# Optimization experiments

Measured on AMD Instinct MI355X. Metric: run time of the kernel, lower is better.

## Reference

```python
import jax, jax.numpy as jnp
import numpy as np

N_NODES = 100000
N_EDGES = 600000
N_RELS = 500
D = 128
RRELU_SLOPE = (1.0 / 8.0 + 1.0 / 3.0) / 2.0  # nn.RReLU eval-mode fixed slope


def setup_inputs() -> dict:
    key = jax.random.key(0)
    ks = jax.random.split(key, 9)
    ent_embed = jax.random.normal(ks[0], (N_NODES, D), dtype=jnp.float32)
    rel_embed = jax.random.normal(ks[1], (N_RELS, D), dtype=jnp.float32)
    W_rel0 = jax.random.normal(ks[2], (D, D), dtype=jnp.float32) * 0.05
    W_loop0 = jax.random.normal(ks[3], (D, D), dtype=jnp.float32) * 0.05
    W_rel1 = jax.random.normal(ks[4], (D, D), dtype=jnp.float32) * 0.05
    W_loop1 = jax.random.normal(ks[5], (D, D), dtype=jnp.float32) * 0.05
    src = jax.random.randint(ks[6], (N_EDGES,), 0, N_NODES, dtype=jnp.int32)
    dst = jax.random.randint(ks[7], (N_EDGES,), 0, N_NODES, dtype=jnp.int32)
    rel_id = jax.random.randint(ks[8], (N_EDGES,), 0, N_RELS, dtype=jnp.int32)
    # standard DGL right-norm: 1 / in-degree per destination node
    deg = jnp.zeros((N_NODES,), dtype=jnp.float32).at[dst].add(1.0)
    norm = (1.0 / jnp.maximum(deg, 1.0))[:, None]  # (N, 1)
    return {
        "ent_embed": ent_embed, "rel_embed": rel_embed, "norm": norm,
        "W_rel0": W_rel0, "W_loop0": W_loop0,
        "W_rel1": W_rel1, "W_loop1": W_loop1,
        "src": src, "dst": dst, "rel_id": rel_id,
    }


def reference(ent_embed, rel_embed, norm, W_rel0, W_loop0, W_rel1, W_loop1, src, dst, rel_id):
    n = ent_embed.shape[0]
    edge_h = rel_embed[rel_id]  # (E, D), set once, reused across layers (as in source)
    h = ent_embed
    for W_rel, W_loop in ((W_rel0, W_loop0), (W_rel1, W_loop1)):
        self_msg = h @ W_loop                      # (N, D)
        msg = (edge_h + h[src]) @ W_rel            # gather src + edge, transform
        agg = jax.ops.segment_sum(msg, dst, num_segments=n)  # scatter-sum to dst
        h = jax.nn.leaky_relu(agg * norm + self_msg, RRELU_SLOPE)
    return h
```

## Files before the change

### kernel.cpp

```cpp
#include <hip/hip_runtime.h>
#include <hip/hip_bf16.h>

#define NN 100000
#define NE 600000
#define DD 128
#define SLOPE 0.22916666666666666f
#define NB1 98
#define SENT ((500u << 17) | 100000u)
#define MAXSLOT 1000448
#define NTILE 6250

typedef __attribute__((ext_vector_type(4))) float f32x4;
typedef __attribute__((ext_vector_type(4))) unsigned u32x4;
typedef __attribute__((ext_vector_type(8))) short s16x8;
typedef __attribute__((ext_vector_type(4))) short s16x4;

__device__ __forceinline__ unsigned short f2b(float f) {
  union { float f; unsigned u; } v; v.f = f;
  unsigned u = v.u;
  return (unsigned short)((u + 0x7fffu + ((u >> 16) & 1u)) >> 16);
}
__device__ __forceinline__ float b2f(short s) {
  union { unsigned u; float f; } v;
  v.u = ((unsigned)(unsigned short)s) << 16;
  return v.f;
}
__device__ __forceinline__ int pdegf(float nm) {
  int d = (int)(1.0f / nm + 0.5f);
  return (d + 3) & ~3;
}

__global__ void prep_all(const float* __restrict__ ent, const float* __restrict__ rel,
                         const float* __restrict__ Wr0, const float* __restrict__ Wl0,
                         const float* __restrict__ Wr1, const float* __restrict__ Wl1,
                         unsigned short* __restrict__ entb, unsigned short* __restrict__ relb,
                         unsigned short* __restrict__ Wt) {
  int i = blockIdx.x * blockDim.x + threadIdx.x;
  if (i < (NN + 1) * 16) {
    s16x8 o = {0, 0, 0, 0, 0, 0, 0, 0};
    if (i < NN * 16) {
      f32x4 v0 = *(const f32x4*)(ent + (size_t)i * 8);
      f32x4 v1 = *(const f32x4*)(ent + (size_t)i * 8 + 4);
      o[0] = (short)f2b(v0[0]); o[1] = (short)f2b(v0[1]);
      o[2] = (short)f2b(v0[2]); o[3] = (short)f2b(v0[3]);
      o[4] = (short)f2b(v1[0]); o[5] = (short)f2b(v1[1]);
      o[6] = (short)f2b(v1[2]); o[7] = (short)f2b(v1[3]);
    }
    *(s16x8*)(entb + (size_t)i * 8) = o;
  }
  if (i < 501 * 16) {
    s16x8 o = {0, 0, 0, 0, 0, 0, 0, 0};
    if (i < 500 * 16) {
      f32x4 v0 = *(const f32x4*)(rel + (size_t)i * 8);
      f32x4 v1 = *(const f32x4*)(rel + (size_t)i * 8 + 4);
      o[0] = (short)f2b(v0[0]); o[1] = (short)f2b(v0[1]);
      o[2] = (short)f2b(v0[2]); o[3] = (short)f2b(v0[3]);
      o[4] = (short)f2b(v1[0]); o[5] = (short)f2b(v1[1]);
      o[6] = (short)f2b(v1[2]); o[7] = (short)f2b(v1[3]);
    }
    *(s16x8*)(relb + (size_t)i * 8) = o;
  }
  if (i < 8192) {
    int L = i >> 12, rem = i & 4095;
    int n = rem >> 9, k = (rem >> 6) & 7, lane = rem & 63;
    int c = n * 16 + (lane & 15);
    int kk0 = k * 32 + (lane >> 4) * 8;
    const float* Wr = L ? Wr1 : Wr0;
    const float* Wl = L ? Wl1 : Wl0;
    s16x8 o;
#pragma unroll
    for (int t = 0; t < 8; t++) {
      int kk = kk0 + t;
      float v = (kk < DD) ? Wr[kk * DD + c] : Wl[(kk - DD) * DD + c];
      o[t] = (short)f2b(v);
    }
    *(s16x8*)(Wt + (size_t)i * 8) = o;
  }
}

__global__ void sentinel_fill(unsigned* __restrict__ epack) {
  int i = blockIdx.x * blockDim.x + threadIdx.x;
  if (i < MAXSLOT / 4) {
    u32x4 s = {SENT, SENT, SENT, SENT};
    *(u32x4*)(epack + (size_t)i * 4) = s;
  }
}

__global__ void scan_a(const float* __restrict__ norm, int* __restrict__ psum) {
  __shared__ int lds[256];
  int b = blockIdx.x, t = threadIdx.x;
  int base = b * 1024 + t * 4;
  int s = 0;
#pragma unroll
  for (int j = 0; j < 4; j++) { int i = base + j; if (i < NN) s += pdegf(norm[i]); }
  lds[t] = s; __syncthreads();
  for (int st = 128; st > 0; st >>= 1) { if (t < st) lds[t] += lds[t + st]; __syncthreads(); }
  if (t == 0) psum[b] = lds[0];
}

__global__ void scan_b(int* __restrict__ psum, int* __restrict__ off) {
  __shared__ int lds[128];
  int t = threadIdx.x;
  lds[t] = (t < NB1) ? psum[t] : 0; __syncthreads();
  for (int st = 1; st < 128; st <<= 1) {
    int v = (t >= st) ? lds[t - st] : 0;
    __syncthreads();
    lds[t] += v;
    __syncthreads();
  }
  if (t == 127) off[NN] = lds[127];
  if (t < NB1) psum[t] = t ? lds[t - 1] : 0;
}

__global__ void scan_c(const float* __restrict__ norm, const int* __restrict__ psum,
                       int* __restrict__ off, int* __restrict__ cur) {
  __shared__ int lds[256];
  int b = blockIdx.x, t = threadIdx.x;
  int base = b * 1024 + t * 4;
  int v[4]; int s = 0;
#pragma unroll
  for (int j = 0; j < 4; j++) { int i = base + j; v[j] = (i < NN) ? pdegf(norm[i]) : 0; s += v[j]; }
  lds[t] = s; __syncthreads();
  for (int st = 1; st < 256; st <<= 1) {
    int u = (t >= st) ? lds[t - st] : 0;
    __syncthreads();
    lds[t] += u;
    __syncthreads();
  }
  int run = (t ? lds[t - 1] : 0) + psum[b];
#pragma unroll
  for (int j = 0; j < 4; j++) {
    int i = base + j;
    if (i < NN) { off[i] = run; cur[i] = run; run += v[j]; }
  }
}

__global__ void fill_pack(const int* __restrict__ src, const int* __restrict__ dst,
                          const int* __restrict__ rid, int* __restrict__ cur,
                          unsigned* __restrict__ epack) {
  int e = blockIdx.x * blockDim.x + threadIdx.x;
  if (e < NE) {
    int slot = atomicAdd(&cur[dst[e]], 1);
    epack[slot] = (unsigned)src[e] | ((unsigned)rid[e] << 17);
  }
}

__global__ void gather1(const unsigned short* __restrict__ hb, const unsigned short* __restrict__ relb,
                        const float* __restrict__ norm, const int* __restrict__ off,
                        const unsigned* __restrict__ epack,
                        unsigned short* __restrict__ preb, unsigned short* __restrict__ relaggn) {
  int gid = blockIdx.x * blockDim.x + threadIdx.x;
  int g = gid >> 5;
  if (g >= NN) return;
  int c = (gid & 31) << 2;
  int beg = off[g], end = off[g + 1];
  float h0 = 0.f, h1 = 0.f, h2 = 0.f, h3 = 0.f;
  float r0 = 0.f, r1 = 0.f, r2 = 0.f, r3 = 0.f;
  for (int e = beg; e < end; e += 4) {
    u32x4 w = *(const u32x4*)(epack + e);
    s16x4 hv[4], rv[4];
#pragma unroll
    for (int j = 0; j < 4; j++) {
      int s = (int)(w[j] & 0x1FFFFu);
      int r = (int)(w[j] >> 17);
      hv[j] = *(const s16x4*)(hb + (size_t)s * DD + c);
      rv[j] = *(const s16x4*)(relb + (size_t)r * DD + c);
    }
#pragma unroll
    for (int j = 0; j < 4; j++) {
      h0 += b2f(hv[j][0]); h1 += b2f(hv[j][1]);
      h2 += b2f(hv[j][2]); h3 += b2f(hv[j][3]);
      r0 += b2f(rv[j][0]); r1 += b2f(rv[j][1]);
      r2 += b2f(rv[j][2]); r3 += b2f(rv[j][3]);
    }
  }
  float nm = norm[g];
  s16x4 p, q;
  p[0] = (short)f2b((h0 + r0) * nm); p[1] = (short)f2b((h1 + r1) * nm);
  p[2] = (short)f2b((h2 + r2) * nm); p[3] = (short)f2b((h3 + r3) * nm);
  q[0] = (short)f2b(r0 * nm); q[1] = (short)f2b(r1 * nm);
  q[2] = (short)f2b(r2 * nm); q[3] = (short)f2b(r3 * nm);
  *(s16x4*)(preb + (size_t)g * DD + c) = p;
  *(s16x4*)(relaggn + (size_t)g * DD + c) = q;
}

__global__ void gather2(const unsigned short* __restrict__ hb, const unsigned short* __restrict__ relaggn,
                        const float* __restrict__ norm, const int* __restrict__ off,
                        const unsigned* __restrict__ epack, unsigned short* __restrict__ preb) {
  int gid = blockIdx.x * blockDim.x + threadIdx.x;
  int g = gid >> 5;
  if (g >= NN) return;
  int c = (gid & 31) << 2;
  int beg = off[g], end = off[g + 1];
  float h0 = 0.f, h1 = 0.f, h2 = 0.f, h3 = 0.f;
  for (int e = beg; e < end; e += 4) {
    u32x4 w = *(const u32x4*)(epack + e);
    s16x4 hv[4];
#pragma unroll
    for (int j = 0; j < 4; j++) {
      int s = (int)(w[j] & 0x1FFFFu);
      hv[j] = *(const s16x4*)(hb + (size_t)s * DD + c);
    }
#pragma unroll
    for (int j = 0; j < 4; j++) {
      h0 += b2f(hv[j][0]); h1 += b2f(hv[j][1]);
      h2 += b2f(hv[j][2]); h3 += b2f(hv[j][3]);
    }
  }
  float nm = norm[g];
  s16x4 ra = *(const s16x4*)(relaggn + (size_t)g * DD + c);
  s16x4 p;
  p[0] = (short)f2b(__builtin_fmaf(h0, nm, b2f(ra[0])));
  p[1] = (short)f2b(__builtin_fmaf(h1, nm, b2f(ra[1])));
  p[2] = (short)f2b(__builtin_fmaf(h2, nm, b2f(ra[2])));
  p[3] = (short)f2b(__builtin_fmaf(h3, nm, b2f(ra[3])));
  *(s16x4*)(preb + (size_t)g * DD + c) = p;
}

template <int OUTF32>
__launch_bounds__(512, 4)
__global__ void layer_mm(const unsigned short* __restrict__ preb, const unsigned short* __restrict__ hb,
                         const unsigned short* __restrict__ Wt, void* __restrict__ outp) {
  __shared__ unsigned short Blds[32768];
  int tid = threadIdx.x;
  int wave = tid >> 6, lane = tid & 63;
  int l16 = lane & 15, lhi = lane >> 4;

  for (int i = tid; i < 4096; i += 512)
    *(s16x8*)(&Blds[(size_t)i * 8]) = *(const s16x8*)(Wt + (size_t)i * 8);
  __syncthreads();

  const unsigned short* Bl = &Blds[lane * 8];

  int gw = blockIdx.x * 8 + wave;
  int t0 = gw, t1 = gw + 4096;
  bool has1 = t1 < NTILE;

  const unsigned short* Ap0 = preb + (size_t)(t0 * 16 + l16) * DD + lhi * 8;
  const unsigned short* Ah0 = hb + (size_t)(t0 * 16 + l16) * DD + lhi * 8;
  s16x8 a0[8], a1[8];
#pragma unroll
  for (int ks = 0; ks < 4; ks++) a0[ks] = *(const s16x8*)(Ap0 + ks * 32);
#pragma unroll
  for (int ks = 0; ks < 4; ks++) a0[4 + ks] = *(const s16x8*)(Ah0 + ks * 32);
  if (has1) {
    const unsigned short* Ap1 = preb + (size_t)(t1 * 16 + l16) * DD + lhi * 8;
    const unsigned short* Ah1 = hb + (size_t)(t1 * 16 + l16) * DD + lhi * 8;
#pragma unroll
    for (int ks = 0; ks < 4; ks++) a1[ks] = *(const s16x8*)(Ap1 + ks * 32);
#pragma unroll
    for (int ks = 0; ks < 4; ks++) a1[4 + ks] = *(const s16x8*)(Ah1 + ks * 32);
  }

  {
    f32x4 acc[8];
#pragma unroll
    for (int n = 0; n < 8; n++) acc[n] = (f32x4){0.f, 0.f, 0.f, 0.f};
#pragma unroll
    for (int n = 0; n < 8; n++) {
#pragma unroll
      for (int k = 0; k < 8; k++) {
        s16x8 b = *(const s16x8*)(Bl + (n * 8 + k) * 512);
        acc[n] = __builtin_amdgcn_mfma_f32_16x16x32_bf16(a0[k], b, acc[n], 0, 0, 0);
      }
    }
    int r0 = t0 * 16;
#pragma unroll
    for (int n = 0; n < 8; n++) {
#pragma unroll
      for (int j = 0; j < 4; j++) {
        int gr = r0 + lhi * 4 + j;
        float x = acc[n][j];
        x = x > 0.f ? x : x * SLOPE;
        if (OUTF32) ((float*)outp)[(size_t)gr * DD + n * 16 + l16] = x;
        else ((unsigned short*)outp)[(size_t)gr * DD + n * 16 + l16] = f2b(x);
      }
    }
  }
  if (has1) {
    f32x4 acc[8];
#pragma unroll
    for (int n = 0; n < 8; n++) acc[n] = (f32x4){0.f, 0.f, 0.f, 0.f};
#pragma unroll
    for (int n = 0; n < 8; n++) {
#pragma unroll
      for (int k = 0; k < 8; k++) {
        s16x8 b = *(const s16x8*)(Bl + (n * 8 + k) * 512);
        acc[n] = __builtin_amdgcn_mfma_f32_16x16x32_bf16(a1[k], b, acc[n], 0, 0, 0);
      }
    }
    int r0 = t1 * 16;
#pragma unroll
    for (int n = 0; n < 8; n++) {
#pragma unroll
      for (int j = 0; j < 4; j++) {
        int gr = r0 + lhi * 4 + j;
        float x = acc[n][j];
        x = x > 0.f ? x : x * SLOPE;
        if (OUTF32) ((float*)outp)[(size_t)gr * DD + n * 16 + l16] = x;
        else ((unsigned short*)outp)[(size_t)gr * DD + n * 16 + l16] = f2b(x);
      }
    }
  }
}

extern "C" void kernel_launch(void* const* d_in, const int* in_sizes, int n_in,
                              void* d_out, int out_size, void* d_ws, size_t ws_size,
                              hipStream_t stream) {
  const float* ent  = (const float*)d_in[0];
  const float* rel  = (const float*)d_in[1];
  const float* norm = (const float*)d_in[2];
  const float* Wr0  = (const float*)d_in[3];
  const float* Wl0  = (const float*)d_in[4];
  const float* Wr1  = (const float*)d_in[5];
  const float* Wl1  = (const float*)d_in[6];
  const int* src = (const int*)d_in[7];
  const int* dst = (const int*)d_in[8];
  const int* rid = (const int*)d_in[9];
  float* out = (float*)d_out;

  char* ws = (char*)d_ws;
  unsigned short* entb    = (unsigned short*)ws;
  unsigned short* preb    = (unsigned short*)(ws + 25600256);
  unsigned short* relaggn = (unsigned short*)(ws + 51200256);
  unsigned short* Wt      = (unsigned short*)(ws + 76800256);
  unsigned short* relb    = (unsigned short*)(ws + 76931328);
  int* off   = (int*)(ws + 77059584);
  int* cur   = (int*)(ws + 77459600);
  int* psum  = (int*)(ws + 77859600);
  unsigned* epack = (unsigned*)(ws + 77860112);

  prep_all<<<((NN + 1) * 16 + 255) / 256, 256, 0, stream>>>(ent, rel, Wr0, Wl0, Wr1, Wl1, entb, relb, Wt);
  sentinel_fill<<<(MAXSLOT / 4 + 255) / 256, 256, 0, stream>>>(epack);

  scan_a<<<NB1, 256, 0, stream>>>(norm, psum);
  scan_b<<<1, 128, 0, stream>>>(psum, off);
  scan_c<<<NB1, 256, 0, stream>>>(norm, psum, off, cur);
  fill_pack<<<(NE + 255) / 256, 256, 0, stream>>>(src, dst, rid, cur, epack);

  const int gb = (NN * 32 + 255) / 256;

  gather1<<<gb, 256, 0, stream>>>(entb, relb, norm, off, epack, preb, relaggn);
  layer_mm<0><<<512, 512, 0, stream>>>(preb, entb, Wt, entb);

  gather2<<<gb, 256, 0, stream>>>(entb, relaggn, norm, off, epack, preb);
  layer_mm<1><<<512, 512, 0, stream>>>(preb, entb, Wt + 32768, out);
}
```

Before: 171.4 us.

## Build CSR edge list via atomicExch linked lists instead of atomic-add slots

```diff
diff --git a/kernel.cpp b/kernel.cpp
--- a/kernel.cpp
+++ b/kernel.cpp
@@ -78,14 +78,6 @@
   }
 }
 
-__global__ void sentinel_fill(unsigned* __restrict__ epack) {
-  int i = blockIdx.x * blockDim.x + threadIdx.x;
-  if (i < MAXSLOT / 4) {
-    u32x4 s = {SENT, SENT, SENT, SENT};
-    *(u32x4*)(epack + (size_t)i * 4) = s;
-  }
-}
-
 __global__ void scan_a(const float* __restrict__ norm, int* __restrict__ psum) {
   __shared__ int lds[256];
   int b = blockIdx.x, t = threadIdx.x;
@@ -113,7 +105,7 @@
 }
 
 __global__ void scan_c(const float* __restrict__ norm, const int* __restrict__ psum,
-                       int* __restrict__ off, int* __restrict__ cur) {
+                       int* __restrict__ off) {
   __shared__ int lds[256];
   int b = blockIdx.x, t = threadIdx.x;
   int base = b * 1024 + t * 4;
@@ -131,18 +123,35 @@
 #pragma unroll
   for (int j = 0; j < 4; j++) {
     int i = base + j;
-    if (i < NN) { off[i] = run; cur[i] = run; run += v[j]; }
-  }
-}
-
-__global__ void fill_pack(const int* __restrict__ src, const int* __restrict__ dst,
-                          const int* __restrict__ rid, int* __restrict__ cur,
-                          unsigned* __restrict__ epack) {
-  int e = blockIdx.x * blockDim.x + threadIdx.x;
-  if (e < NE) {
-    int slot = atomicAdd(&cur[dst[e]], 1);
-    epack[slot] = (unsigned)src[e] | ((unsigned)rid[e] << 17);
-  }
+    if (i < NN) { off[i] = run; run += v[j]; }
+  }
+}
+
+__global__ void link_build(const int* __restrict__ dst, int* __restrict__ head,
+                           int* __restrict__ nxt) {
+  int i = blockIdx.x * blockDim.x + threadIdx.x;
+  int e0 = i * 2;
+  if (e0 + 1 < NE) {
+    int d0 = dst[e0], d1 = dst[e0 + 1];
+    nxt[e0] = atomicExch(&head[d0], e0);
+    nxt[e0 + 1] = atomicExch(&head[d1], e0 + 1);
+  } else if (e0 < NE) {
+    nxt[e0] = atomicExch(&head[dst[e0]], e0);
+  }
+}
+
+__global__ void compact(const int* __restrict__ head, const int* __restrict__ nxt,
+                        const int* __restrict__ src, const int* __restrict__ rid,
+                        const int* __restrict__ off, unsigned* __restrict__ epack) {
+  int g = blockIdx.x * blockDim.x + threadIdx.x;
+  if (g >= NN) return;
+  int slot = off[g], endp = off[g + 1];
+  int e = head[g];
+  while (e >= 0) {
+    epack[slot++] = (unsigned)src[e] | ((unsigned)rid[e] << 17);
+    e = nxt[e];
+  }
+  while (slot < endp) epack[slot++] = SENT;
 }
 
 __global__ void gather1(const unsigned short* __restrict__ hb, const unsigned short* __restrict__ relb,
@@ -326,17 +335,19 @@
   unsigned short* Wt      = (unsigned short*)(ws + 76800256);
   unsigned short* relb    = (unsigned short*)(ws + 76931328);
   int* off   = (int*)(ws + 77059584);
-  int* cur   = (int*)(ws + 77459600);
+  int* head  = (int*)(ws + 77459600);
   int* psum  = (int*)(ws + 77859600);
   unsigned* epack = (unsigned*)(ws + 77860112);
+  int* nxt   = (int*)relaggn;
 
   prep_all<<<((NN + 1) * 16 + 255) / 256, 256, 0, stream>>>(ent, rel, Wr0, Wl0, Wr1, Wl1, entb, relb, Wt);
-  sentinel_fill<<<(MAXSLOT / 4 + 255) / 256, 256, 0, stream>>>(epack);
-
+
+  hipMemsetAsync(head, 0xFF, (size_t)NN * 4, stream);
+  link_build<<<(NE / 2 + 255) / 256, 256, 0, stream>>>(dst, head, nxt);
   scan_a<<<NB1, 256, 0, stream>>>(norm, psum);
   scan_b<<<1, 128, 0, stream>>>(psum, off);
-  scan_c<<<NB1, 256, 0, stream>>>(norm, psum, off, cur);
-  fill_pack<<<(NE + 255) / 256, 256, 0, stream>>>(src, dst, rid, cur, epack);
+  scan_c<<<NB1, 256, 0, stream>>>(norm, psum, off);
+  compact<<<(NN + 255) / 256, 256, 0, stream>>>(head, nxt, src, rid, off, epack);
 
   const int gb = (NN * 32 + 255) / 256;
 
```

Result: slower. 185.0 us (+7.9%).

## Replace global-atomic edge bucketing with two-pass binned scatter and LDS sort

Applied to the files above, without the earlier changes.

```diff
diff --git a/kernel.cpp b/kernel.cpp
--- a/kernel.cpp
+++ b/kernel.cpp
@@ -7,8 +7,10 @@
 #define SLOPE 0.22916666666666666f
 #define NB1 98
 #define SENT ((500u << 17) | 100000u)
-#define MAXSLOT 1000448
 #define NTILE 6250
+#define NBKT 196
+#define EPB 2048
+#define CAP 12288
 
 typedef __attribute__((ext_vector_type(4))) float f32x4;
 typedef __attribute__((ext_vector_type(4))) unsigned u32x4;
@@ -78,14 +80,6 @@
   }
 }
 
-__global__ void sentinel_fill(unsigned* __restrict__ epack) {
-  int i = blockIdx.x * blockDim.x + threadIdx.x;
-  if (i < MAXSLOT / 4) {
-    u32x4 s = {SENT, SENT, SENT, SENT};
-    *(u32x4*)(epack + (size_t)i * 4) = s;
-  }
-}
-
 __global__ void scan_a(const float* __restrict__ norm, int* __restrict__ psum) {
   __shared__ int lds[256];
   int b = blockIdx.x, t = threadIdx.x;
@@ -113,7 +107,7 @@
 }
 
 __global__ void scan_c(const float* __restrict__ norm, const int* __restrict__ psum,
-                       int* __restrict__ off, int* __restrict__ cur) {
+                       int* __restrict__ off) {
   __shared__ int lds[256];
   int b = blockIdx.x, t = threadIdx.x;
   int base = b * 1024 + t * 4;
@@ -131,17 +125,74 @@
 #pragma unroll
   for (int j = 0; j < 4; j++) {
     int i = base + j;
-    if (i < NN) { off[i] = run; cur[i] = run; run += v[j]; }
-  }
-}
-
-__global__ void fill_pack(const int* __restrict__ src, const int* __restrict__ dst,
-                          const int* __restrict__ rid, int* __restrict__ cur,
-                          unsigned* __restrict__ epack) {
-  int e = blockIdx.x * blockDim.x + threadIdx.x;
-  if (e < NE) {
-    int slot = atomicAdd(&cur[dst[e]], 1);
-    epack[slot] = (unsigned)src[e] | ((unsigned)rid[e] << 17);
+    if (i < NN) { off[i] = run; run += v[j]; }
+  }
+}
+
+__global__ void bin_scatter(const int* __restrict__ src, const int* __restrict__ dst,
+                            const int* __restrict__ rid, int* __restrict__ bktcur,
+                            unsigned* __restrict__ sval, unsigned short* __restrict__ sdst) {
+  __shared__ int hist[NBKT];
+  __shared__ int base[NBKT];
+  __shared__ int rnk[NBKT];
+  int tid = threadIdx.x;
+  int e0 = blockIdx.x * EPB;
+  for (int t = tid; t < NBKT; t += 256) hist[t] = 0;
+  __syncthreads();
+  int d[8];
+#pragma unroll
+  for (int j = 0; j < 8; j++) {
+    int idx = tid + j * 256;
+    int e = e0 + idx;
+    d[j] = (e < NE) ? dst[e] : -1;
+    if (d[j] >= 0) atomicAdd(&hist[d[j] >> 9], 1);
+  }
+  __syncthreads();
+  for (int t = tid; t < NBKT; t += 256) {
+    base[t] = hist[t] ? atomicAdd(&bktcur[t], hist[t]) : 0;
+    rnk[t] = 0;
+  }
+  __syncthreads();
+#pragma unroll
+  for (int j = 0; j < 8; j++) {
+    if (d[j] >= 0) {
+      int e = e0 + tid + j * 256;
+      int b = d[j] >> 9;
+      int r = atomicAdd(&rnk[b], 1);
+      int pos = base[b] + r;
+      if (pos < CAP) {
+        sval[(size_t)b * CAP + pos] = (unsigned)src[e] | ((unsigned)rid[e] << 17);
+        sdst[(size_t)b * CAP + pos] = (unsigned short)(d[j] & 511);
+      }
+    }
+  }
+}
+
+__global__ void bin_sort(const int* __restrict__ bktcur, const unsigned* __restrict__ sval,
+                         const unsigned short* __restrict__ sdst, const int* __restrict__ off,
+                         unsigned* __restrict__ epack) {
+  __shared__ int cur[512];
+  int b = blockIdx.x, tid = threadIdx.x;
+  int g0 = b << 9;
+  for (int t = tid; t < 512; t += 256) {
+    int g = g0 + t;
+    cur[t] = (g < NN) ? off[g] : 0;
+  }
+  __syncthreads();
+  int scnt = min(bktcur[b], CAP);
+  for (int i = tid; i < scnt; i += 256) {
+    unsigned v = sval[(size_t)b * CAP + i];
+    int gl = sdst[(size_t)b * CAP + i];
+    int pos = atomicAdd(&cur[gl], 1);
+    epack[pos] = v;
+  }
+  __syncthreads();
+  for (int t = tid; t < 512; t += 256) {
+    int g = g0 + t;
+    if (g < NN) {
+      int s = cur[t], e = off[g + 1];
+      for (; s < e; s++) epack[s] = SENT;
+    }
   }
 }
 
@@ -326,17 +377,21 @@
   unsigned short* Wt      = (unsigned short*)(ws + 76800256);
   unsigned short* relb    = (unsigned short*)(ws + 76931328);
   int* off   = (int*)(ws + 77059584);
-  int* cur   = (int*)(ws + 77459600);
-  int* psum  = (int*)(ws + 77859600);
-  unsigned* epack = (unsigned*)(ws + 77860112);
+  int* bktcur = (int*)(ws + 77459600);
+  int* psum  = (int*)(ws + 77860384);
+  unsigned* epack = (unsigned*)(ws + 77860896);
+  unsigned* sval = (unsigned*)relaggn;
+  unsigned short* sdst = (unsigned short*)(ws + 51200256 + 9633792);
 
   prep_all<<<((NN + 1) * 16 + 255) / 256, 256, 0, stream>>>(ent, rel, Wr0, Wl0, Wr1, Wl1, entb, relb, Wt);
-  sentinel_fill<<<(MAXSLOT / 4 + 255) / 256, 256, 0, stream>>>(epack);
 
   scan_a<<<NB1, 256, 0, stream>>>(norm, psum);
   scan_b<<<1, 128, 0, stream>>>(psum, off);
-  scan_c<<<NB1, 256, 0, stream>>>(norm, psum, off, cur);
-  fill_pack<<<(NE + 255) / 256, 256, 0, stream>>>(src, dst, rid, cur, epack);
+  scan_c<<<NB1, 256, 0, stream>>>(norm, psum, off);
+
+  hipMemsetAsync(bktcur, 0, NBKT * 4, stream);
+  bin_scatter<<<(NE + EPB - 1) / EPB, 256, 0, stream>>>(src, dst, rid, bktcur, sval, sdst);
+  bin_sort<<<NBKT, 256, 0, stream>>>(bktcur, sval, sdst, off, epack);
 
   const int gb = (NN * 32 + 255) / 256;
 
```

After: 160.8 us. 1.07x faster.
